# Kernel optimization log

Measured on AMD Instinct MI355X. Metric: run time of the kernel, lower is better.

Reference implementation:

```python
import jax, jax.numpy as jnp
import numpy as np

NUM_GRAPHS = 8
N_NODES = 100000


def setup_inputs() -> dict:
    key = jax.random.key(0)
    ks = jax.random.split(key, 8)
    d = 64
    E = 1600000
    x = jax.random.normal(ks[0], (N_NODES, d), dtype=jnp.float32)
    # nn.Linear weights (out,in) with std=0.1 init per GNNlayer; biases zero
    W1 = 0.1 * jax.random.normal(ks[1], (d, d), dtype=jnp.float32)
    W2 = 0.1 * jax.random.normal(ks[2], (d, d), dtype=jnp.float32)
    W3 = 0.1 * jax.random.normal(ks[3], (d, d), dtype=jnp.float32)
    b1 = jnp.zeros((d,), dtype=jnp.float32)
    b2 = jnp.zeros((d,), dtype=jnp.float32)
    b3 = jnp.zeros((d,), dtype=jnp.float32)
    src = jax.random.randint(ks[4], (E,), 0, N_NODES, dtype=jnp.int32)
    dst = jax.random.randint(ks[5], (E,), 0, N_NODES, dtype=jnp.int32)
    node2graph = jnp.sort(jax.random.randint(ks[6], (N_NODES,), 0, NUM_GRAPHS, dtype=jnp.int32))
    return {"x": x, "W1": W1, "b1": b1, "W2": W2, "b2": b2,
            "W3": W3, "b3": b3, "src": src, "dst": dst, "node2graph": node2graph}


def _gnn_layer(h, W, b, src, dst):
    # GNNlayer: per-node linear, then copy_u -> sum reduce at dst
    m = h @ W.T + b                       # [N, d]
    msg = m[src]                          # [E, d] edge gather
    return jax.ops.segment_sum(msg, dst, num_segments=N_NODES)  # [N, d]


def reference(x, W1, b1, W2, b2, W3, b3, src, dst, node2graph):
    h = jnp.tanh(_gnn_layer(x, W1, b1, src, dst))
    h = jnp.tanh(_gnn_layer(h, W2, b2, src, dst))
    H_feat = _gnn_layer(h, W3, b3, src, dst)      # [N, out_dim]
    # dgl.unbatch + per-graph sum of all node features -> scalar per graph
    node_scalar = jnp.sum(H_feat, axis=-1)        # [N]
    per_graph = jax.ops.segment_sum(node_scalar, node2graph, num_segments=NUM_GRAPHS)
    return per_graph[None, :]                     # [1, num_graphs]
```

## Files before the change

### kernel.cpp

```cpp
#include <hip/hip_runtime.h>
#include <math.h>

#define NGRAPHS 8
#define KBSHIFT 8
#define BSZ 256
#define KMAX 512
#define BSTRIDE 6144
#define PCHUNK 3125

typedef _Float16 h2 __attribute__((ext_vector_type(2)));
typedef _Float16 v8hf __attribute__((ext_vector_type(8)));
typedef float f32x4 __attribute__((ext_vector_type(4)));

__device__ __forceinline__ h2 as_h2(unsigned u) { return __builtin_bit_cast(h2, u); }
__device__ __forceinline__ unsigned as_u(h2 h) { return __builtin_bit_cast(unsigned, h); }
__device__ __forceinline__ unsigned pkf16(float a, float b) {
    auto v = __builtin_amdgcn_cvt_pkrtz(a, b);
    return __builtin_bit_cast(unsigned, v);
}
__device__ __forceinline__ float ftanh(float x) {
    float t = __expf(2.0f * x);
    return 1.0f - 2.0f * __builtin_amdgcn_rcpf(t + 1.0f);
}

template<bool TANH, bool ZB>
__global__ __launch_bounds__(256) void gemm_kernel(
    const float* __restrict__ in_, const float* __restrict__ W,
    const float* __restrict__ bias, unsigned* __restrict__ out,
    int* __restrict__ bcursor, int N)
{
    __shared__ union {
        struct { uint4 Wc[512]; uint4 Xc[512]; } s;
        float Cf[64 * 68];
    } u;
    const int t = threadIdx.x;
    const int node0 = blockIdx.x * 64;
    if (ZB && blockIdx.x == 0) { bcursor[t] = 0; bcursor[t + 256] = 0; }

    const float4* W4 = (const float4*)W;
    #pragma unroll
    for (int k = 0; k < 2; ++k) {
        int idx = k * 256 + t;
        int o = idx >> 3, ch = idx & 7;
        float4 w0 = W4[idx * 2];
        float4 w1 = W4[idx * 2 + 1];
        u.s.Wc[o * 8 + (ch ^ (o & 7))] =
            make_uint4(pkf16(w0.x, w0.y), pkf16(w0.z, w0.w),
                       pkf16(w1.x, w1.y), pkf16(w1.z, w1.w));
    }
    {
        const float4* in4 = (const float4*)in_ + (size_t)node0 * 16;
        #pragma unroll
        for (int k = 0; k < 2; ++k) {
            int idx = k * 256 + t;
            int nl = idx >> 3, ch = idx & 7;
            float4 a0 = make_float4(0.f, 0.f, 0.f, 0.f);
            float4 a1 = make_float4(0.f, 0.f, 0.f, 0.f);
            if (node0 + nl < N) { a0 = in4[idx * 2]; a1 = in4[idx * 2 + 1]; }
            if (TANH) {
                a0.x = ftanh(a0.x); a0.y = ftanh(a0.y); a0.z = ftanh(a0.z); a0.w = ftanh(a0.w);
                a1.x = ftanh(a1.x); a1.y = ftanh(a1.y); a1.z = ftanh(a1.z); a1.w = ftanh(a1.w);
            }
            u.s.Xc[nl * 8 + (ch ^ (nl & 7))] =
                make_uint4(pkf16(a0.x, a0.y), pkf16(a0.z, a0.w),
                           pkf16(a1.x, a1.y), pkf16(a1.z, a1.w));
        }
    }
    __syncthreads();

    const int w = t >> 6, l = t & 63;
    const int lo = l & 15, kb = l >> 4, sx = lo & 7;
    const v8hf* Xv = (const v8hf*)u.s.Xc;
    const v8hf* Wv = (const v8hf*)u.s.Wc;
    const int arow = (w * 16 + lo) * 8;
    v8hf a0 = Xv[arow + (kb ^ sx)];
    v8hf a1 = Xv[arow + ((4 + kb) ^ sx)];
    f32x4 acc[4];
    #pragma unroll
    for (int i = 0; i < 4; ++i) acc[i] = (f32x4){0.f, 0.f, 0.f, 0.f};
    #pragma unroll
    for (int ct = 0; ct < 4; ++ct) {
        const int brow = (ct * 16 + lo) * 8;
        v8hf b0 = Wv[brow + (kb ^ sx)];
        v8hf b1 = Wv[brow + ((4 + kb) ^ sx)];
        acc[ct] = __builtin_amdgcn_mfma_f32_16x16x32_f16(a0, b0, acc[ct], 0, 0, 0);
        acc[ct] = __builtin_amdgcn_mfma_f32_16x16x32_f16(a1, b1, acc[ct], 0, 0, 0);
    }
    __syncthreads();

    #pragma unroll
    for (int ct = 0; ct < 4; ++ct) {
        #pragma unroll
        for (int j = 0; j < 4; ++j)
            u.Cf[(w * 16 + kb * 4 + j) * 68 + ct * 16 + lo] = acc[ct][j];
    }
    __syncthreads();

    {
        const int nl = t >> 2, seg = t & 3;
        if (node0 + nl < N) {
            const float* cp = &u.Cf[nl * 68 + seg * 16];
            float4 c0 = *(const float4*)(cp);
            float4 c1 = *(const float4*)(cp + 4);
            float4 c2 = *(const float4*)(cp + 8);
            float4 c3 = *(const float4*)(cp + 12);
            const float4* b4 = (const float4*)bias + seg * 4;
            float4 e0 = b4[0], e1 = b4[1], e2 = b4[2], e3 = b4[3];
            uint4 o0 = make_uint4(pkf16(c0.x + e0.x, c0.y + e0.y), pkf16(c0.z + e0.z, c0.w + e0.w),
                                  pkf16(c1.x + e1.x, c1.y + e1.y), pkf16(c1.z + e1.z, c1.w + e1.w));
            uint4 o1 = make_uint4(pkf16(c2.x + e2.x, c2.y + e2.y), pkf16(c2.z + e2.z, c2.w + e2.w),
                                  pkf16(c3.x + e3.x, c3.y + e3.y), pkf16(c3.z + e3.z, c3.w + e3.w));
            uint4* op = (uint4*)out + (size_t)(node0 + nl) * 8 + seg * 2;
            op[0] = o0;
            op[1] = o1;
        }
    }
}

__global__ __launch_bounds__(256) void gather_gemm_kernel(
    const uint4* __restrict__ m, const int* __restrict__ esrc,
    const int* __restrict__ rowptr, const int* __restrict__ rowend,
    const float* __restrict__ W, const float* __restrict__ bias,
    unsigned* __restrict__ out, int N)
{
    __shared__ union {
        struct { uint4 Wc[512]; uint4 Xc[512]; } s;
        float Cf[64 * 68];
    } u;
    const int t = threadIdx.x;
    const int node0 = blockIdx.x * 64;

    const float4* W4 = (const float4*)W;
    #pragma unroll
    for (int k = 0; k < 2; ++k) {
        int idx = k * 256 + t;
        int o = idx >> 3, ch = idx & 7;
        float4 w0 = W4[idx * 2];
        float4 w1 = W4[idx * 2 + 1];
        u.s.Wc[o * 8 + (ch ^ (o & 7))] =
            make_uint4(pkf16(w0.x, w0.y), pkf16(w0.z, w0.w),
                       pkf16(w1.x, w1.y), pkf16(w1.z, w1.w));
    }

    const int grp = t >> 5, l32 = t & 31;
    const int sub = l32 >> 3, c = l32 & 7;
    for (int i = 0; i < 8; ++i) {
        const int nl = grp * 8 + i;
        const int n = node0 + nl;
        h2 a0 = {0, 0}, a1 = {0, 0}, a2 = {0, 0}, a3 = {0, 0};
        if (n < N) {
            int beg = rowptr[n], end = rowend[n];
            int e = beg + sub;
            for (; e + 4 < end; e += 8) {
                int sA = esrc[e], sB = esrc[e + 4];
                uint4 vA = m[(size_t)sA * 8 + c];
                uint4 vB = m[(size_t)sB * 8 + c];
                a0 += as_h2(vA.x); a1 += as_h2(vA.y);
                a2 += as_h2(vA.z); a3 += as_h2(vA.w);
                a0 += as_h2(vB.x); a1 += as_h2(vB.y);
                a2 += as_h2(vB.z); a3 += as_h2(vB.w);
            }
            if (e < end) {
                uint4 vA = m[(size_t)esrc[e] * 8 + c];
                a0 += as_h2(vA.x); a1 += as_h2(vA.y);
                a2 += as_h2(vA.z); a3 += as_h2(vA.w);
            }
        }
        #pragma unroll
        for (int d = 8; d <= 16; d <<= 1) {
            a0 += as_h2(__shfl_xor(as_u(a0), d));
            a1 += as_h2(__shfl_xor(as_u(a1), d));
            a2 += as_h2(__shfl_xor(as_u(a2), d));
            a3 += as_h2(__shfl_xor(as_u(a3), d));
        }
        if (sub == 0) {
            float f0 = ftanh((float)a0.x), f1 = ftanh((float)a0.y);
            float f2 = ftanh((float)a1.x), f3 = ftanh((float)a1.y);
            float f4 = ftanh((float)a2.x), f5 = ftanh((float)a2.y);
            float f6 = ftanh((float)a3.x), f7 = ftanh((float)a3.y);
            u.s.Xc[nl * 8 + (c ^ (nl & 7))] =
                make_uint4(pkf16(f0, f1), pkf16(f2, f3), pkf16(f4, f5), pkf16(f6, f7));
        }
    }
    __syncthreads();

    const int w = t >> 6, l = t & 63;
    const int lo = l & 15, kb = l >> 4, sx = lo & 7;
    const v8hf* Xv = (const v8hf*)u.s.Xc;
    const v8hf* Wv = (const v8hf*)u.s.Wc;
    const int arow = (w * 16 + lo) * 8;
    v8hf a0 = Xv[arow + (kb ^ sx)];
    v8hf a1 = Xv[arow + ((4 + kb) ^ sx)];
    f32x4 acc[4];
    #pragma unroll
    for (int i = 0; i < 4; ++i) acc[i] = (f32x4){0.f, 0.f, 0.f, 0.f};
    #pragma unroll
    for (int ct = 0; ct < 4; ++ct) {
        const int brow = (ct * 16 + lo) * 8;
        v8hf b0 = Wv[brow + (kb ^ sx)];
        v8hf b1 = Wv[brow + ((4 + kb) ^ sx)];
        acc[ct] = __builtin_amdgcn_mfma_f32_16x16x32_f16(a0, b0, acc[ct], 0, 0, 0);
        acc[ct] = __builtin_amdgcn_mfma_f32_16x16x32_f16(a1, b1, acc[ct], 0, 0, 0);
    }
    __syncthreads();

    #pragma unroll
    for (int ct = 0; ct < 4; ++ct) {
        #pragma unroll
        for (int j = 0; j < 4; ++j)
            u.Cf[(w * 16 + kb * 4 + j) * 68 + ct * 16 + lo] = acc[ct][j];
    }
    __syncthreads();

    {
        const int nl = t >> 2, seg = t & 3;
        if (node0 + nl < N) {
            const float* cp = &u.Cf[nl * 68 + seg * 16];
            float4 c0 = *(const float4*)(cp);
            float4 c1 = *(const float4*)(cp + 4);
            float4 c2 = *(const float4*)(cp + 8);
            float4 c3 = *(const float4*)(cp + 12);
            const float4* b4 = (const float4*)bias + seg * 4;
            float4 e0 = b4[0], e1 = b4[1], e2 = b4[2], e3 = b4[3];
            uint4 o0 = make_uint4(pkf16(c0.x + e0.x, c0.y + e0.y), pkf16(c0.z + e0.z, c0.w + e0.w),
                                  pkf16(c1.x + e1.x, c1.y + e1.y), pkf16(c1.z + e1.z, c1.w + e1.w));
            uint4 o1 = make_uint4(pkf16(c2.x + e2.x, c2.y + e2.y), pkf16(c2.z + e2.z, c2.w + e2.w),
                                  pkf16(c3.x + e3.x, c3.y + e3.y), pkf16(c3.z + e3.z, c3.w + e3.w));
            uint4* op = (uint4*)out + (size_t)(node0 + nl) * 8 + seg * 2;
            op[0] = o0;
            op[1] = o1;
        }
    }
}

__global__ __launch_bounds__(512) void partition_kernel(
    const int* __restrict__ src, const int* __restrict__ dst,
    int* __restrict__ bcursor, unsigned* __restrict__ pairs, int E, int K)
{
    __shared__ int h[512];
    __shared__ int sh[512];
    __shared__ int base[512];
    __shared__ int cur[512];
    __shared__ unsigned val[PCHUNK + 3];
    __shared__ unsigned short bk[PCHUNK + 3];
    const int t = threadIdx.x;
    const int lo = blockIdx.x * PCHUNK;
    int hi = lo + PCHUNK; if (hi > E) hi = E;
    const int cnt = hi - lo;

    h[t] = 0; cur[t] = 0;
    __syncthreads();
    for (int e = lo + t; e < hi; e += 512)
        atomicAdd(&h[dst[e] >> KBSHIFT], 1);
    __syncthreads();
    int v = h[t];
    int x = v;
    #pragma unroll
    for (int off = 1; off < 512; off <<= 1) {
        int u = (t >= off) ? h[t - off] : 0;
        __syncthreads();
        x += u;
        h[t] = x;
        __syncthreads();
    }
    sh[t] = x - v;
    base[t] = (t < K && v > 0) ? atomicAdd(&bcursor[t], v) : 0;
    __syncthreads();
    for (int e = lo + t; e < hi; e += 512) {
        int d = dst[e];
        int k = d >> KBSHIFT;
        int pos = atomicAdd(&cur[k], 1);
        int j = sh[k] + pos;
        val[j] = ((unsigned)(d & (BSZ - 1)) << 23) | (unsigned)src[e];
        bk[j] = (unsigned short)k;
    }
    __syncthreads();
    for (int j = t; j < cnt; j += 512) {
        int k = bk[j];
        int idx = base[k] + (j - sh[k]);
        if (idx < BSTRIDE)
            pairs[(size_t)k * BSTRIDE + idx] = val[j];
    }
}

__global__ __launch_bounds__(256) void bucket_build_kernel(
    const unsigned* __restrict__ pairs, const int* __restrict__ bcursor,
    int* __restrict__ rowptr, int* __restrict__ rowend, int* __restrict__ esrc,
    const float* __restrict__ W3, const float* __restrict__ b3,
    float* __restrict__ w3s, int N)
{
    __shared__ int cnt[BSZ];
    __shared__ int tmp[BSZ];
    __shared__ int cur[BSZ];
    const int k = blockIdx.x;
    const int t = threadIdx.x;
    const int ebase = k * BSTRIDE;
    int ec = bcursor[k]; if (ec > BSTRIDE) ec = BSTRIDE;
    const int eend = ebase + ec;

    cnt[t] = 0;
    __syncthreads();
    for (int e = ebase + t; e < eend; e += BSZ)
        atomicAdd(&cnt[pairs[e] >> 23], 1);
    __syncthreads();

    int v = cnt[t];
    tmp[t] = v;
    __syncthreads();
    #pragma unroll
    for (int off = 1; off < BSZ; off <<= 1) {
        int u = (t >= off) ? tmp[t - off] : 0;
        __syncthreads();
        tmp[t] += u;
        __syncthreads();
    }
    int excl = tmp[t] - v;
    cur[t] = excl;
    int n = (k << KBSHIFT) + t;
    if (n < N) {
        rowptr[n] = ebase + excl;
        rowend[n] = ebase + excl + v;
    }
    __syncthreads();

    for (int e = ebase + t; e < eend; e += BSZ) {
        unsigned p = pairs[e];
        int pos = atomicAdd(&cur[p >> 23], 1);
        esrc[ebase + pos] = (int)(p & 0x7fffffu);
    }

    if (k == 0) {
        if (t < 64) {
            float s = 0.f;
            for (int o = 0; o < 64; ++o) s += W3[o * 64 + t];
            w3s[t] = s;
        }
        if (t == 64) {
            float bs = 0.f;
            for (int j = 0; j < 64; ++j) bs += b3[j];
            w3s[64] = bs;
        }
    }
}

__global__ __launch_bounds__(256) void gather_s3_kernel(
    const uint4* __restrict__ m, const int* __restrict__ esrc,
    const int* __restrict__ rowptr, const int* __restrict__ rowend,
    const float* __restrict__ w3s, float* __restrict__ s3,
    float* __restrict__ outz, int N)
{
    const int t = threadIdx.x;
    if (blockIdx.x == 0 && t < NGRAPHS) outz[t] = 0.f;
    const int n = blockIdx.x * 8 + (t >> 5);
    const int l32 = t & 31;
    const int sub = l32 >> 3, c = l32 & 7;
    h2 a0 = {0, 0}, a1 = {0, 0}, a2 = {0, 0}, a3 = {0, 0};
    if (n < N) {
        int beg = rowptr[n], end = rowend[n];
        int e = beg + sub;
        for (; e + 4 < end; e += 8) {
            int sA = esrc[e], sB = esrc[e + 4];
            uint4 vA = m[(size_t)sA * 8 + c];
            uint4 vB = m[(size_t)sB * 8 + c];
            a0 += as_h2(vA.x); a1 += as_h2(vA.y);
            a2 += as_h2(vA.z); a3 += as_h2(vA.w);
            a0 += as_h2(vB.x); a1 += as_h2(vB.y);
            a2 += as_h2(vB.z); a3 += as_h2(vB.w);
        }
        if (e < end) {
            uint4 vA = m[(size_t)esrc[e] * 8 + c];
            a0 += as_h2(vA.x); a1 += as_h2(vA.y);
            a2 += as_h2(vA.z); a3 += as_h2(vA.w);
        }
    }
    #pragma unroll
    for (int d = 8; d <= 16; d <<= 1) {
        a0 += as_h2(__shfl_xor(as_u(a0), d));
        a1 += as_h2(__shfl_xor(as_u(a1), d));
        a2 += as_h2(__shfl_xor(as_u(a2), d));
        a3 += as_h2(__shfl_xor(as_u(a3), d));
    }
    float4 w0 = ((const float4*)w3s)[c * 2];
    float4 w1 = ((const float4*)w3s)[c * 2 + 1];
    float partial = ftanh((float)a0.x) * w0.x + ftanh((float)a0.y) * w0.y
                  + ftanh((float)a1.x) * w0.z + ftanh((float)a1.y) * w0.w
                  + ftanh((float)a2.x) * w1.x + ftanh((float)a2.y) * w1.y
                  + ftanh((float)a3.x) * w1.z + ftanh((float)a3.y) * w1.w;
    partial += __shfl_xor(partial, 1);
    partial += __shfl_xor(partial, 2);
    partial += __shfl_xor(partial, 4);
    if (l32 == 0 && n < N) s3[n] = partial + w3s[64];
}

__global__ __launch_bounds__(256) void graph_reduce_kernel(
    const float* __restrict__ s3, const int* __restrict__ esrc,
    const int* __restrict__ bcursor,
    const int* __restrict__ rowptr, const int* __restrict__ rowend,
    const int* __restrict__ n2g, float* __restrict__ out, int N)
{
    __shared__ float red[NGRAPHS];
    const int k = blockIdx.x;
    const int t = threadIdx.x;
    const int ebase = k * BSTRIDE;
    int ec = bcursor[k]; if (ec > BSTRIDE) ec = BSTRIDE;
    const int n0 = k << KBSHIFT;
    const int nlast = ((n0 + BSZ) < N ? (n0 + BSZ) : N) - 1;
    const int g0 = n2g[n0], g1 = n2g[nlast];

    if (g0 == g1) {
        float acc = 0.f;
        for (int e = ebase + t; e < ebase + ec; e += 256) acc += s3[esrc[e]];
        #pragma unroll
        for (int d = 1; d < 64; d <<= 1) acc += __shfl_xor(acc, d);
        if ((t & 63) == 0) red[t >> 6] = acc;
        __syncthreads();
        if (t == 0)
            unsafeAtomicAdd(&out[g0], red[0] + red[1] + red[2] + red[3]);
    } else {
        if (t < NGRAPHS) red[t] = 0.f;
        __syncthreads();
        const int n = n0 + t;
        if (n < N) {
            float acc = 0.f;
            for (int e = rowptr[n]; e < rowend[n]; ++e) acc += s3[esrc[e]];
            atomicAdd(&red[n2g[n]], acc);
        }
        __syncthreads();
        if (t < NGRAPHS) unsafeAtomicAdd(&out[t], red[t]);
    }
}

extern "C" void kernel_launch(void* const* d_in, const int* in_sizes, int n_in,
                              void* d_out, int out_size, void* d_ws, size_t ws_size,
                              hipStream_t stream)
{
    const float* x   = (const float*)d_in[0];
    const float* W1  = (const float*)d_in[1];
    const float* b1  = (const float*)d_in[2];
    const float* W2  = (const float*)d_in[3];
    const float* b2  = (const float*)d_in[4];
    const float* W3  = (const float*)d_in[5];
    const float* b3  = (const float*)d_in[6];
    const int*   src = (const int*)d_in[7];
    const int*   dst = (const int*)d_in[8];
    const int*   n2g = (const int*)d_in[9];

    const int N = in_sizes[0] / 64;
    const int E = in_sizes[7];
    const int K = (N + BSZ - 1) >> KBSHIFT;

    char* p = (char*)d_ws;
    auto carve = [&](size_t bytes) {
        char* r = p;
        p += (bytes + 255) & ~(size_t)255;
        return r;
    };
    unsigned* A     = (unsigned*)carve((size_t)N * 64 * 2);
    unsigned* B     = (unsigned*)carve((size_t)N * 64 * 2);
    float* s3b      = (float*)carve((size_t)N * sizeof(float));
    float* w3s      = (float*)carve(65 * sizeof(float));
    int*   bcursor  = (int*)carve(KMAX * sizeof(int));
    int*   rowptr   = (int*)carve((size_t)N * sizeof(int));
    int*   rowend   = (int*)carve((size_t)N * sizeof(int));
    int*   esrc     = (int*)carve((size_t)K * BSTRIDE * sizeof(int));
    unsigned* pairs = (unsigned*)B;
    float* out      = (float*)d_out;

    const int gemm_blocks = (N + 63) / 64;
    const int gath_blocks = (N + 7) / 8;
    const int part_blocks = (E + PCHUNK - 1) / PCHUNK;

    gemm_kernel<false, true><<<gemm_blocks, 256, 0, stream>>>(x, W1, b1, A, bcursor, N);

    partition_kernel<<<part_blocks, 512, 0, stream>>>(src, dst, bcursor, pairs, E, K);
    bucket_build_kernel<<<K, BSZ, 0, stream>>>(pairs, bcursor, rowptr, rowend,
                                               esrc, W3, b3, w3s, N);

    gather_gemm_kernel<<<gemm_blocks, 256, 0, stream>>>(
        (const uint4*)A, esrc, rowptr, rowend, W2, b2, B, N);

    gather_s3_kernel<<<gath_blocks, 256, 0, stream>>>(
        (const uint4*)B, esrc, rowptr, rowend, w3s, s3b, out, N);

    graph_reduce_kernel<<<K, 256, 0, stream>>>(s3b, esrc, bcursor,
                                               rowptr, rowend, n2g, out, N);
}
```

Before: 207.7 us.

## Fuse first GEMM and edge partitioning into one heterogeneous-block kernel

Merges the layer-1 GEMM and the edge partition pass into a single launch. The first PB blocks do partitioning and the remaining blocks each do two 64-node GEMM tiles, with shared memory unioned across both roles. The bcursor zeroing moves to a hipMemsetAsync, since the partition blocks no longer run after the GEMM in stream order. bucket_build now stages each bucket's pairs in LDS so the second pass reads shared memory instead of global. The aim is less launch overhead and overlap of two independent stages, at the cost of extra memset work and heavier LDS use per block, which may reduce occupancy.

```diff
diff --git a/kernel.cpp b/kernel.cpp
--- a/kernel.cpp
+++ b/kernel.cpp
@@ -23,19 +23,68 @@
     return 1.0f - 2.0f * __builtin_amdgcn_rcpf(t + 1.0f);
 }
 
-template<bool TANH, bool ZB>
-__global__ __launch_bounds__(256) void gemm_kernel(
+__global__ __launch_bounds__(512) void gemm_part_kernel(
     const float* __restrict__ in_, const float* __restrict__ W,
     const float* __restrict__ bias, unsigned* __restrict__ out,
-    int* __restrict__ bcursor, int N)
+    const int* __restrict__ src, const int* __restrict__ dst,
+    int* __restrict__ bcursor, unsigned* __restrict__ pairs,
+    int E, int K, int N, int PB)
 {
     __shared__ union {
-        struct { uint4 Wc[512]; uint4 Xc[512]; } s;
-        float Cf[64 * 68];
+        struct { struct { uint4 Wc[512]; uint4 Xc[512]; } tile[2]; } g;
+        struct { float Cf[2][64 * 68]; } e;
+        struct { int h[512], sh[512], base[512], cur[512];
+                 unsigned val[PCHUNK + 3];
+                 unsigned short bk[PCHUNK + 3]; } p;
     } u;
-    const int t = threadIdx.x;
-    const int node0 = blockIdx.x * 64;
-    if (ZB && blockIdx.x == 0) { bcursor[t] = 0; bcursor[t + 256] = 0; }
+    const int bid = blockIdx.x;
+    const int t512 = threadIdx.x;
+
+    if (bid < PB) {
+        const int t = t512;
+        const int lo = bid * PCHUNK;
+        int hi = lo + PCHUNK; if (hi > E) hi = E;
+        const int cnt = hi - lo;
+
+        u.p.h[t] = 0; u.p.cur[t] = 0;
+        __syncthreads();
+        for (int e = lo + t; e < hi; e += 512)
+            atomicAdd(&u.p.h[dst[e] >> KBSHIFT], 1);
+        __syncthreads();
+        int v = u.p.h[t];
+        int x = v;
+        #pragma unroll
+        for (int off = 1; off < 512; off <<= 1) {
+            int q = (t >= off) ? u.p.h[t - off] : 0;
+            __syncthreads();
+            x += q;
+            u.p.h[t] = x;
+            __syncthreads();
+        }
+        u.p.sh[t] = x - v;
+        u.p.base[t] = (t < K && v > 0) ? atomicAdd(&bcursor[t], v) : 0;
+        __syncthreads();
+        for (int e = lo + t; e < hi; e += 512) {
+            int d = dst[e];
+            int k = d >> KBSHIFT;
+            int pos = atomicAdd(&u.p.cur[k], 1);
+            int j = u.p.sh[k] + pos;
+            u.p.val[j] = ((unsigned)(d & (BSZ - 1)) << 23) | (unsigned)src[e];
+            u.p.bk[j] = (unsigned short)k;
+        }
+        __syncthreads();
+        for (int j = t; j < cnt; j += 512) {
+            int k = u.p.bk[j];
+            int idx = u.p.base[k] + (j - u.p.sh[k]);
+            if (idx < BSTRIDE)
+                pairs[(size_t)k * BSTRIDE + idx] = u.p.val[j];
+        }
+        return;
+    }
+
+    const int half = t512 >> 8, t = t512 & 255;
+    const int node0 = (bid - PB) * 128 + half * 64;
+    auto& S = u.g.tile[half];
 
     const float4* W4 = (const float4*)W;
     #pragma unroll
@@ -44,7 +93,7 @@
         int o = idx >> 3, ch = idx & 7;
         float4 w0 = W4[idx * 2];
         float4 w1 = W4[idx * 2 + 1];
-        u.s.Wc[o * 8 + (ch ^ (o & 7))] =
+        S.Wc[o * 8 + (ch ^ (o & 7))] =
             make_uint4(pkf16(w0.x, w0.y), pkf16(w0.z, w0.w),
                        pkf16(w1.x, w1.y), pkf16(w1.z, w1.w));
     }
@@ -57,11 +106,7 @@
             float4 a0 = make_float4(0.f, 0.f, 0.f, 0.f);
             float4 a1 = make_float4(0.f, 0.f, 0.f, 0.f);
             if (node0 + nl < N) { a0 = in4[idx * 2]; a1 = in4[idx * 2 + 1]; }
-            if (TANH) {
-                a0.x = ftanh(a0.x); a0.y = ftanh(a0.y); a0.z = ftanh(a0.z); a0.w = ftanh(a0.w);
-                a1.x = ftanh(a1.x); a1.y = ftanh(a1.y); a1.z = ftanh(a1.z); a1.w = ftanh(a1.w);
-            }
-            u.s.Xc[nl * 8 + (ch ^ (nl & 7))] =
+            S.Xc[nl * 8 + (ch ^ (nl & 7))] =
                 make_uint4(pkf16(a0.x, a0.y), pkf16(a0.z, a0.w),
                            pkf16(a1.x, a1.y), pkf16(a1.z, a1.w));
         }
@@ -70,8 +115,8 @@
 
     const int w = t >> 6, l = t & 63;
     const int lo = l & 15, kb = l >> 4, sx = lo & 7;
-    const v8hf* Xv = (const v8hf*)u.s.Xc;
-    const v8hf* Wv = (const v8hf*)u.s.Wc;
+    const v8hf* Xv = (const v8hf*)S.Xc;
+    const v8hf* Wv = (const v8hf*)S.Wc;
     const int arow = (w * 16 + lo) * 8;
     v8hf a0 = Xv[arow + (kb ^ sx)];
     v8hf a1 = Xv[arow + ((4 + kb) ^ sx)];
@@ -88,18 +133,19 @@
     }
     __syncthreads();
 
+    float* Cf = u.e.Cf[half];
     #pragma unroll
     for (int ct = 0; ct < 4; ++ct) {
         #pragma unroll
         for (int j = 0; j < 4; ++j)
-            u.Cf[(w * 16 + kb * 4 + j) * 68 + ct * 16 + lo] = acc[ct][j];
+            Cf[(w * 16 + kb * 4 + j) * 68 + ct * 16 + lo] = acc[ct][j];
     }
     __syncthreads();
 
     {
         const int nl = t >> 2, seg = t & 3;
         if (node0 + nl < N) {
-            const float* cp = &u.Cf[nl * 68 + seg * 16];
+            const float* cp = &Cf[nl * 68 + seg * 16];
             float4 c0 = *(const float4*)(cp);
             float4 c1 = *(const float4*)(cp + 4);
             float4 c2 = *(const float4*)(cp + 8);
@@ -233,56 +279,6 @@
     }
 }
 
-__global__ __launch_bounds__(512) void partition_kernel(
-    const int* __restrict__ src, const int* __restrict__ dst,
-    int* __restrict__ bcursor, unsigned* __restrict__ pairs, int E, int K)
-{
-    __shared__ int h[512];
-    __shared__ int sh[512];
-    __shared__ int base[512];
-    __shared__ int cur[512];
-    __shared__ unsigned val[PCHUNK + 3];
-    __shared__ unsigned short bk[PCHUNK + 3];
-    const int t = threadIdx.x;
-    const int lo = blockIdx.x * PCHUNK;
-    int hi = lo + PCHUNK; if (hi > E) hi = E;
-    const int cnt = hi - lo;
-
-    h[t] = 0; cur[t] = 0;
-    __syncthreads();
-    for (int e = lo + t; e < hi; e += 512)
-        atomicAdd(&h[dst[e] >> KBSHIFT], 1);
-    __syncthreads();
-    int v = h[t];
-    int x = v;
-    #pragma unroll
-    for (int off = 1; off < 512; off <<= 1) {
-        int u = (t >= off) ? h[t - off] : 0;
-        __syncthreads();
-        x += u;
-        h[t] = x;
-        __syncthreads();
-    }
-    sh[t] = x - v;
-    base[t] = (t < K && v > 0) ? atomicAdd(&bcursor[t], v) : 0;
-    __syncthreads();
-    for (int e = lo + t; e < hi; e += 512) {
-        int d = dst[e];
-        int k = d >> KBSHIFT;
-        int pos = atomicAdd(&cur[k], 1);
-        int j = sh[k] + pos;
-        val[j] = ((unsigned)(d & (BSZ - 1)) << 23) | (unsigned)src[e];
-        bk[j] = (unsigned short)k;
-    }
-    __syncthreads();
-    for (int j = t; j < cnt; j += 512) {
-        int k = bk[j];
-        int idx = base[k] + (j - sh[k]);
-        if (idx < BSTRIDE)
-            pairs[(size_t)k * BSTRIDE + idx] = val[j];
-    }
-}
-
 __global__ __launch_bounds__(256) void bucket_build_kernel(
     const unsigned* __restrict__ pairs, const int* __restrict__ bcursor,
     int* __restrict__ rowptr, int* __restrict__ rowend, int* __restrict__ esrc,
@@ -292,16 +288,19 @@
     __shared__ int cnt[BSZ];
     __shared__ int tmp[BSZ];
     __shared__ int cur[BSZ];
+    __shared__ unsigned sp[BSTRIDE];
     const int k = blockIdx.x;
     const int t = threadIdx.x;
     const int ebase = k * BSTRIDE;
     int ec = bcursor[k]; if (ec > BSTRIDE) ec = BSTRIDE;
-    const int eend = ebase + ec;
 
     cnt[t] = 0;
     __syncthreads();
-    for (int e = ebase + t; e < eend; e += BSZ)
-        atomicAdd(&cnt[pairs[e] >> 23], 1);
+    for (int j = t; j < ec; j += BSZ) {
+        unsigned p = pairs[ebase + j];
+        sp[j] = p;
+        atomicAdd(&cnt[p >> 23], 1);
+    }
     __syncthreads();
 
     int v = cnt[t];
@@ -309,9 +308,9 @@
     __syncthreads();
     #pragma unroll
     for (int off = 1; off < BSZ; off <<= 1) {
-        int u = (t >= off) ? tmp[t - off] : 0;
-        __syncthreads();
-        tmp[t] += u;
+        int q = (t >= off) ? tmp[t - off] : 0;
+        __syncthreads();
+        tmp[t] += q;
         __syncthreads();
     }
     int excl = tmp[t] - v;
@@ -323,8 +322,8 @@
     }
     __syncthreads();
 
-    for (int e = ebase + t; e < eend; e += BSZ) {
-        unsigned p = pairs[e];
+    for (int j = t; j < ec; j += BSZ) {
+        unsigned p = sp[j];
         int pos = atomicAdd(&cur[p >> 23], 1);
         esrc[ebase + pos] = (int)(p & 0x7fffffu);
     }
@@ -466,13 +465,15 @@
     unsigned* pairs = (unsigned*)B;
     float* out      = (float*)d_out;
 
+    const int PB = (E + PCHUNK - 1) / PCHUNK;
+    const int GB = (N + 127) / 128;
     const int gemm_blocks = (N + 63) / 64;
     const int gath_blocks = (N + 7) / 8;
-    const int part_blocks = (E + PCHUNK - 1) / PCHUNK;
-
-    gemm_kernel<false, true><<<gemm_blocks, 256, 0, stream>>>(x, W1, b1, A, bcursor, N);
-
-    partition_kernel<<<part_blocks, 512, 0, stream>>>(src, dst, bcursor, pairs, E, K);
+
+    hipMemsetAsync(bcursor, 0, KMAX * sizeof(int), stream);
+    gemm_part_kernel<<<PB + GB, 512, 0, stream>>>(
+        x, W1, b1, A, src, dst, bcursor, pairs, E, K, N, PB);
+
     bucket_build_kernel<<<K, BSZ, 0, stream>>>(pairs, bcursor, rowptr, rowend,
                                                esrc, W3, b3, w3s, N);
 
```

Result: no change. 204.7 us (-1.5%).
